# Kernel optimization log

Measured on AMD Instinct MI355X. Metric: run time of the kernel, lower is better.

Reference implementation:

```python
import jax, jax.numpy as jnp
import numpy as np

B, L, DIM, H, D, WS = 2, 2048, 1024, 16, 64, 256
SCALE = D ** -0.5


def _rope_tables(seq_len, dim, dtype):
    inv_freq = 1.0 / (10000.0 ** (jnp.arange(0, dim, 2, dtype=jnp.float32) / dim))
    t = jnp.arange(seq_len, dtype=jnp.float32)
    freqs = jnp.einsum('i,j->ij', t, inv_freq)          # [L, D/2]
    emb = jnp.concatenate([freqs, freqs], axis=-1)       # [L, D]
    return jnp.cos(emb).astype(dtype), jnp.sin(emb).astype(dtype)


def _rotate_half(x):
    x1, x2 = x[..., : x.shape[-1] // 2], x[..., x.shape[-1] // 2:]
    return jnp.concatenate([-x2, x1], axis=-1)


def _apply_rope(t, cos, sin):
    # t: [B, L, H, D]; cos/sin: [L, D] broadcast over batch and heads
    return t * cos[None, :, None, :] + _rotate_half(t) * sin[None, :, None, :]


def setup_inputs() -> dict:
    key = jax.random.key(0)
    k0, k1, k2 = jax.random.split(key, 3)
    x = jax.random.normal(k0, (B, L, DIM), dtype=jnp.float32)
    Wqkv = jax.random.normal(k1, (3 * H * D, DIM), dtype=jnp.float32) * 0.02
    bqkv = jnp.zeros((3 * H * D,), dtype=jnp.float32)
    Wproj = jax.random.normal(k2, (DIM, H * D), dtype=jnp.float32) * 0.02
    bproj = jnp.zeros((DIM,), dtype=jnp.float32)
    return {"x": x, "Wqkv": Wqkv, "bqkv": bqkv, "Wproj": Wproj, "bproj": bproj, "is_global": 1}


def _attention(x, Wqkv, bqkv, Wproj, bproj, is_global):
    b, l, _ = x.shape
    qkv = x @ Wqkv.T + bqkv                              # [B, L, 3*H*D]
    q, k, v = jnp.split(qkv, 3, axis=-1)
    q, k, v = (t.reshape(b, l, H, D) for t in (q, k, v))
    cos, sin = _rope_tables(l, D, x.dtype)
    q = _apply_rope(q, cos, sin)
    k = _apply_rope(k, cos, sin)
    if is_global:
        attn = jnp.einsum('bshd,bthd->bhst', q, k) * SCALE
        attn = jax.nn.softmax(attn, axis=-1)
        out = jnp.einsum('bhst,bthd->bshd', attn, v)     # [B, L, H, D]
    else:
        pad = (WS - l % WS) % WS
        if pad > 0:
            q, k, v = (jnp.pad(t, ((0, 0), (0, pad), (0, 0), (0, 0))) for t in (q, k, v))
        w = (l + pad) // WS
        q = q.reshape(b, w, WS, H, D)
        k = k.reshape(b, w, WS, H, D)
        v = v.reshape(b, w, WS, H, D)
        attn = jnp.einsum('bwshd,bwthd->bwhst', q, k) * SCALE
        attn = jax.nn.softmax(attn, axis=-1)
        out = jnp.einsum('bwhst,bwthd->bwshd', attn, v).reshape(b, w * WS, H, D)
        out = out[:, :l]
    return out.reshape(b, l, H * D) @ Wproj.T + bproj


def reference(x, Wqkv, bqkv, Wproj, bproj, is_global):
    return _attention(x, Wqkv, bqkv, Wproj, bproj, is_global)
```

## Files before the change

### kernel.cpp

```cpp
#include <hip/hip_runtime.h>
#include <math.h>

#define NB 2
#define NL 2048
#define NDIM 1024
#define NH 16
#define ND 64
#define NWS 256
#define NM (NB*NL)
#define QSCALE 0.18033688011112042f

typedef __attribute__((ext_vector_type(8))) short short8;
typedef __attribute__((ext_vector_type(4))) float f32x4;
typedef unsigned short ushort_t;
typedef unsigned int uint_t;

#define MFMA16(a,b,acc) __builtin_amdgcn_mfma_f32_16x16x32_bf16((a),(b),(acc),0,0,0)

static __device__ __forceinline__ ushort_t f2bf(float x){
    uint_t u = __float_as_uint(x);
    uint_t r = (u + 0x7fff + ((u >> 16) & 1)) >> 16;
    return (ushort_t)r;
}
static __device__ __forceinline__ float bf2f(ushort_t u){
    return __uint_as_float(((uint_t)u) << 16);
}
static __device__ __forceinline__ float fast_exp2(float x){
#if __has_builtin(__builtin_amdgcn_exp2f)
    return __builtin_amdgcn_exp2f(x);
#else
    return exp2f(x);
#endif
}

static __device__ __forceinline__ void async_load16(const void* g, void* l){
    __builtin_amdgcn_global_load_lds(
        (const __attribute__((address_space(1))) unsigned int*)g,
        (__attribute__((address_space(3))) unsigned int*)l, 16, 0, 0);
}

__launch_bounds__(256)
__global__ void split_all(const float* __restrict__ x,  ushort_t* __restrict__ xh,  ushort_t* __restrict__ xl,
                          const float* __restrict__ wq, ushort_t* __restrict__ wqh, ushort_t* __restrict__ wql,
                          const float* __restrict__ wp, ushort_t* __restrict__ wph, ushort_t* __restrict__ wpl)
{
    int i = blockIdx.x*256 + threadIdx.x;
    const float* in; ushort_t *oh, *ol;
    if (i < 1048576)      { in = x;  oh = xh;  ol = xl;  }
    else if (i < 1835008) { in = wq; oh = wqh; ol = wql; i -= 1048576; }
    else                  { in = wp; oh = wph; ol = wpl; i -= 1835008; }
    const int e = i*4;
    const float4 v = *(const float4*)(in + e);
    ushort_t h0=f2bf(v.x), h1=f2bf(v.y), h2=f2bf(v.z), h3=f2bf(v.w);
    ushort4 h4; h4.x=h0; h4.y=h1; h4.z=h2; h4.w=h3;
    ushort4 l4;
    l4.x=f2bf(v.x - bf2f(h0)); l4.y=f2bf(v.y - bf2f(h1));
    l4.z=f2bf(v.z - bf2f(h2)); l4.w=f2bf(v.w - bf2f(h3));
    *(ushort4*)(oh + e) = h4;
    *(ushort4*)(ol + e) = l4;
}

__launch_bounds__(256)
__global__ void rope_tab(float* __restrict__ tc, float* __restrict__ ts)
{
    const int idx = blockIdx.x*256 + threadIdx.x;
    const int j = idx >> 11, l = idx & (NL-1);
    const float invf = 1.0f / powf(10000.0f, (float)j * (1.0f/32.0f));
    float s, c;
    sincosf((float)l * invf, &s, &c);
    tc[idx] = c; ts[idx] = s;
}

__launch_bounds__(256, 3)
__global__ void gemm_qkv(const ushort_t* __restrict__ Ah, const ushort_t* __restrict__ Al,
                         const ushort_t* __restrict__ Bh,
                         const float* __restrict__ bias,
                         ushort_t* __restrict__ oQh, ushort_t* __restrict__ oKh,
                         ushort_t* __restrict__ oVth,
                         const float* __restrict__ tcos, const float* __restrict__ tsin)
{
    __shared__ __align__(16) char smem[50176];
    ushort_t* sA_h = (ushort_t*)smem;
    ushort_t* sA_l = (ushort_t*)(smem + 8192);
    ushort_t* sB_h = (ushort_t*)(smem + 16384);
    ushort_t* sBounce = (ushort_t*)smem;
    const int ebuf = 12288;
    const int bbuf = 24576;

    const int tid  = threadIdx.x;
    const int wv   = tid >> 6, lane = tid & 63;
    const int quad = lane >> 4, l16 = lane & 15;
    const int m0 = blockIdx.y << 7, n0 = blockIdx.x << 7;
    const int wr = wv >> 1, wc = wv & 1;

    const ushort_t* gsrc;
    ushort_t* lds_base;
    int rowb, npass;
    if (wv == 0)      { gsrc = Ah; lds_base = sA_h; rowb = m0; npass = 8; }
    else if (wv == 1) { gsrc = Al; lds_base = sA_l; rowb = m0; npass = 8; }
    else { gsrc = Bh; lds_base = sB_h + (wv-2)*64*32; rowb = n0 + (wv-2)*64; npass = 4; }
    const int rl = lane >> 2;
    const int cp = lane & 3;
    const int cg = cp ^ ((rl >> 1) & 3);
    const ushort_t* gptr = gsrc + (size_t)(rowb + rl)*NDIM + cg*8;

    f32x4 acc[4][4];
    #pragma unroll
    for (int i=0;i<4;++i)
        #pragma unroll
        for (int j=0;j<4;++j) acc[i][j] = (f32x4){0.f,0.f,0.f,0.f};

    const int swz = (l16 >> 1) & 3;
    const int ac_off = (wr*64 + l16)*32 + ((quad ^ swz) << 3);
    const int bc_off = (wc*64 + l16)*32 + ((quad ^ swz) << 3);

#define QSTAGE(BUF, KOFF) do { \
        const ushort_t* gp_ = gptr + (KOFF); \
        for (int p=0; p<npass; ++p) \
            async_load16(gp_ + (size_t)p*16*NDIM, (char*)lds_base + (BUF)*bbuf + p*1024); \
    } while(0)

#define QCOMP(BUF) do { \
        const int eo_ = (BUF)*ebuf; \
        short8 ah[4], al[4], bh[4]; \
        _Pragma("unroll") \
        for (int t=0;t<4;++t){ \
            ah[t] = *(const short8*)&sA_h[eo_ + t*512 + ac_off]; \
            al[t] = *(const short8*)&sA_l[eo_ + t*512 + ac_off]; \
            bh[t] = *(const short8*)&sB_h[eo_ + t*512 + bc_off]; \
        } \
        _Pragma("unroll") \
        for (int mt=0;mt<4;++mt) \
            _Pragma("unroll") \
            for (int nt=0;nt<4;++nt){ \
                f32x4 a_ = acc[mt][nt]; \
                a_ = MFMA16(ah[mt], bh[nt], a_); \
                a_ = MFMA16(al[mt], bh[nt], a_); \
                acc[mt][nt] = a_; \
            } \
    } while(0)

    QSTAGE(0, 0);
    for (int k0 = 0; k0 < NDIM; k0 += 64) {
        __syncthreads();
        QSTAGE(1, k0 + 32);
        QCOMP(0);
        __syncthreads();
        if (k0 + 64 < NDIM) QSTAGE(0, k0 + 64);
        QCOMP(1);
    }
#undef QSTAGE
#undef QCOMP

    const int colb = n0 + wc*64;
    const int sel  = colb >> 10;
    const int head = (colb & 1023) >> 6;
    float bq[4];
    #pragma unroll
    for (int nt=0;nt<4;++nt) bq[nt] = bias[colb + nt*16 + l16];

    if (sel == 2) {
        __syncthreads();
        const int bb = m0 >> 11;
        const int Lb = (m0 & (NL-1)) + wr*64;
        ushort_t* sT = sBounce + wv*(64*72);
        const size_t gb = ((size_t)(bb*NH + head)*ND)*NL + Lb;
        const int drow = lane >> 3, dcol = lane & 7;
        #pragma unroll
        for (int mt=0;mt<4;++mt)
            #pragma unroll
            for (int nt=0;nt<4;++nt)
                #pragma unroll
                for (int r=0;r<4;++r)
                    sT[(nt*16+l16)*72 + mt*16 + quad*4 + r] = f2bf(acc[mt][nt][r] + bq[nt]);
        #pragma unroll
        for (int dd=0; dd<8; ++dd){
            const int d = dd*8 + drow;
            const uint4 v = *(const uint4*)&sT[d*72 + dcol*8];
            *(uint4*)(oVth + gb + (size_t)d*NL + dcol*8) = v;
        }
    } else {
        ushort_t* dh = sel ? oKh : oQh;
        const float qs = sel ? 1.0f : QSCALE;
        #pragma unroll
        for (int mt=0;mt<4;++mt)
            #pragma unroll
            for (int r=0;r<4;++r){
                const int m = m0 + wr*64 + mt*16 + quad*4 + r;
                const int bb = m >> 11, l = m & (NL-1);
                const size_t ro = ((size_t)((bb*NH + head)*NL + l)) << 6;
                #pragma unroll
                for (int ntp=0;ntp<2;++ntp){
                    const int j = ntp*16 + l16;
                    const float c = tcos[j*NL + l];
                    const float s = tsin[j*NL + l];
                    const float x1 = acc[mt][ntp  ][r] + bq[ntp];
                    const float x2 = acc[mt][ntp+2][r] + bq[ntp+2];
                    const int d1 = ntp*16 + l16;
                    dh[ro + d1]      = f2bf((x1*c - x2*s) * qs);
                    dh[ro + d1 + 32] = f2bf((x2*c + x1*s) * qs);
                }
            }
    }
}

__launch_bounds__(256, 2)
__global__ void gemm_proj(const ushort_t* __restrict__ Ah, const ushort_t* __restrict__ Al,
                          const ushort_t* __restrict__ Bh, const ushort_t* __restrict__ Bl,
                          const float* __restrict__ bias,
                          float* __restrict__ Cout)
{
    __shared__ __align__(16) char smem[74752];
    ushort_t* sA_h = (ushort_t*)smem;
    ushort_t* sA_l = (ushort_t*)(smem + 8192);
    ushort_t* sB_h = (ushort_t*)(smem + 16384);
    ushort_t* sB_l = (ushort_t*)(smem + 20480);
    const int ebuf = 12288;
    const int bbuf = 24576;

    const int tid  = threadIdx.x;
    const int wv   = tid >> 6, lane = tid & 63;
    const int quad = lane >> 4, l16 = lane & 15;
    const int m0 = blockIdx.y << 7, n0 = blockIdx.x << 6;
    const int wr = wv >> 1, wc = wv & 1;

    const int rl = lane >> 2;
    const int cp = lane & 3;
    const int cg = cp ^ ((rl >> 1) & 3);
    const ushort_t* pAh = Ah + (size_t)(m0 + 32*wv + rl)*NDIM + cg*8;
    const ushort_t* pAl = Al + (size_t)(m0 + 32*wv + rl)*NDIM + cg*8;
    const ushort_t* pBh = Bh + (size_t)(n0 + 16*wv + rl)*NDIM + cg*8;
    const ushort_t* pBl = Bl + (size_t)(n0 + 16*wv + rl)*NDIM + cg*8;
    char* dA  = smem + wv*2048;
    char* dB0 = smem + 16384 + wv*1024;
    char* dB1 = smem + 20480 + wv*1024;

    f32x4 acc[4][2];
    #pragma unroll
    for (int i=0;i<4;++i)
        #pragma unroll
        for (int j=0;j<2;++j) acc[i][j] = (f32x4){0.f,0.f,0.f,0.f};

    const int swz = (l16 >> 1) & 3;
    const int ac_off = (wr*64 + l16)*32 + ((quad ^ swz) << 3);
    const int bc_off = (wc*32 + l16)*32 + ((quad ^ swz) << 3);

#define PSTAGE(SLOT, KOFF) do { \
        const int so_ = (SLOT)*bbuf; \
        async_load16(pAh + (KOFF),           dA + so_); \
        async_load16(pAh + 16*NDIM + (KOFF), dA + so_ + 1024); \
        async_load16(pAl + (KOFF),           dA + so_ + 8192); \
        async_load16(pAl + 16*NDIM + (KOFF), dA + so_ + 9216); \
        async_load16(pBh + (KOFF), dB0 + so_); \
        async_load16(pBl + (KOFF), dB1 + so_); \
    } while(0)

#define PCOMP(SLOT) do { \
        const int eo_ = (SLOT)*ebuf; \
        short8 ah[4], al[4], bh[2], bl[2]; \
        _Pragma("unroll") \
        for (int t=0;t<4;++t){ \
            ah[t] = *(const short8*)&sA_h[eo_ + t*512 + ac_off]; \
            al[t] = *(const short8*)&sA_l[eo_ + t*512 + ac_off]; \
        } \
        _Pragma("unroll") \
        for (int t=0;t<2;++t){ \
            bh[t] = *(const short8*)&sB_h[eo_ + t*512 + bc_off]; \
            bl[t] = *(const short8*)&sB_l[eo_ + t*512 + bc_off]; \
        } \
        _Pragma("unroll") \
        for (int mt=0;mt<4;++mt) \
            _Pragma("unroll") \
            for (int nt=0;nt<2;++nt){ \
                f32x4 a_ = acc[mt][nt]; \
                a_ = MFMA16(ah[mt], bh[nt], a_); \
                a_ = MFMA16(al[mt], bh[nt], a_); \
                a_ = MFMA16(ah[mt], bl[nt], a_); \
                acc[mt][nt] = a_; \
            } \
    } while(0)

#define PPHASE(SLOT, K0, VN) do { \
        asm volatile("s_waitcnt vmcnt(" #VN ")" ::: "memory"); \
        __builtin_amdgcn_sched_barrier(0); \
        __builtin_amdgcn_s_barrier(); \
        __builtin_amdgcn_sched_barrier(0); \
        PCOMP(SLOT); \
        asm volatile("s_waitcnt lgkmcnt(0)" ::: "memory"); \
        __builtin_amdgcn_sched_barrier(0); \
        __builtin_amdgcn_s_barrier(); \
        __builtin_amdgcn_sched_barrier(0); \
        if ((K0) + 96 < NDIM) PSTAGE(SLOT, (K0) + 96); \
    } while(0)

    PSTAGE(0, 0); PSTAGE(1, 32); PSTAGE(2, 64);
    for (int k0 = 0; k0 < 960; k0 += 96) {
        PPHASE(0, k0,      12);
        PPHASE(1, k0 + 32, 12);
        PPHASE(2, k0 + 64, 12);
    }
    PPHASE(0, 960, 0);
    PPHASE(1, 992, 0);
#undef PSTAGE
#undef PCOMP
#undef PPHASE

    const int colb = n0 + wc*32;
    float bq[2];
    #pragma unroll
    for (int nt=0;nt<2;++nt) bq[nt] = bias[colb + nt*16 + l16];
    #pragma unroll
    for (int mt=0;mt<4;++mt)
        #pragma unroll
        for (int r=0;r<4;++r){
            const int m = m0 + wr*64 + mt*16 + quad*4 + r;
            float* orow = Cout + (size_t)m*NDIM + colb;
            #pragma unroll
            for (int nt=0;nt<2;++nt)
                orow[nt*16 + l16] = acc[mt][nt][r] + bq[nt];
        }
}

__launch_bounds__(256, 4)
__global__ void attn_mfma(const ushort_t* __restrict__ Qh,
                          const ushort_t* __restrict__ Kh,
                          const ushort_t* __restrict__ Vth,
                          ushort_t* __restrict__ AOh, ushort_t* __restrict__ AOl,
                          const int* __restrict__ isg)
{
    __shared__ __align__(16) char smem[40960];

    const int tid  = threadIdx.x;
    const int wv   = tid >> 6, lane = tid & 63;
    const int quad = lane >> 4, l16 = lane & 15;
    const int bh = blockIdx.x & 31, qt = blockIdx.x >> 5;
    const int q0w = qt*64 + wv*16;

    short8 bq0, bq1;
    {
        const size_t rb = (((size_t)bh*NL + q0w) << 6) + (size_t)(l16 << 6) + quad*8;
        bq0 = *(const short8*)(Qh + rb);
        bq1 = *(const short8*)(Qh + rb + 32);
    }
    short8 ones;
    #pragma unroll
    for (int j=0;j<8;++j) ones[j] = (short)0x3F80;

    f32x4 o[4];
    #pragma unroll
    for (int dnt=0; dnt<4; ++dnt) o[dnt] = (f32x4){0.f,0.f,0.f,0.f};
    f32x4 lsacc = (f32x4){0.f,0.f,0.f,0.f};

    const int gflag = isg[0];
    int klo, khi;
    if (gflag) { klo = 0; khi = NL; }
    else       { klo = (qt >> 2)*NWS; khi = klo + NWS; }

    const int swz4 = (l16 & 7) << 4;
    const int KC0 = l16*128 + (( quad*16      ) ^ swz4);
    const int KC1 = l16*128 + (( quad*16 + 64 ) ^ swz4);
    const int sPb = 32768 + wv*2048;
    int PW[4];
    #pragma unroll
    for (int knt=0; knt<4; ++knt)
        PW[knt] = sPb + l16*128 + ((knt*32 + quad*8) ^ swz4);
    const int PR0 = sPb + KC0;
    const int PR1 = sPb + KC1;

    const int r8  = lane >> 3;
    const int c8s = (lane & 7) ^ r8;
    const ushort_t* Kp = Kh + (((size_t)bh*NL) << 6)
                       + (size_t)(klo + wv*16 + r8)*64 + c8s*8;
    const ushort_t* Vp = Vth + (size_t)bh*ND*NL
                       + (size_t)(wv*16 + r8)*NL + klo + c8s*8;
    const int kdst = wv*2048;
    const int vdst = 16384 + wv*2048;

#define STAGE(BUF) do { \
        async_load16(Kp,          smem + (BUF)*8192 + kdst); \
        async_load16(Kp + 512,    smem + (BUF)*8192 + kdst + 1024); \
        async_load16(Vp,          smem + (BUF)*8192 + vdst); \
        async_load16(Vp + 8*NL,   smem + (BUF)*8192 + vdst + 1024); \
        Kp += 64*64; Vp += 64; } while (0)

#define TILE(BUF) do { \
        const char* kb_ = smem + (BUF)*8192; \
        const char* vb_ = smem + 16384 + (BUF)*8192; \
        f32x4 s_[4]; \
        _Pragma("unroll") \
        for (int knt=0; knt<4; ++knt) { \
            const short8 a0 = *(const short8*)(kb_ + knt*2048 + KC0); \
            const short8 a1 = *(const short8*)(kb_ + knt*2048 + KC1); \
            f32x4 t = (f32x4){0.f,0.f,0.f,0.f}; \
            t = MFMA16(a0, bq0, t); \
            t = MFMA16(a1, bq1, t); \
            s_[knt] = t; \
        } \
        _Pragma("unroll") \
        for (int knt=0; knt<4; ++knt) { \
            const uint_t u0 = __float_as_uint(fast_exp2(s_[knt][0])); \
            const uint_t u1 = __float_as_uint(fast_exp2(s_[knt][1])); \
            const uint_t u2 = __float_as_uint(fast_exp2(s_[knt][2])); \
            const uint_t u3 = __float_as_uint(fast_exp2(s_[knt][3])); \
            uint2 pk_; \
            pk_.x = __builtin_amdgcn_perm(u1, u0, 0x07060302u); \
            pk_.y = __builtin_amdgcn_perm(u3, u2, 0x07060302u); \
            *(uint2*)(smem + PW[knt]) = pk_; \
        } \
        const short8 fp0 = *(const short8*)(smem + PR0); \
        const short8 fp1 = *(const short8*)(smem + PR1); \
        lsacc = MFMA16(fp0, ones, lsacc); \
        lsacc = MFMA16(fp1, ones, lsacc); \
        _Pragma("unroll") \
        for (int dnt=0; dnt<4; ++dnt) { \
            const short8 v0 = *(const short8*)(vb_ + dnt*2048 + KC0); \
            const short8 v1 = *(const short8*)(vb_ + dnt*2048 + KC1); \
            f32x4 t = o[dnt]; \
            t = MFMA16(fp0, v0, t); \
            t = MFMA16(fp1, v1, t); \
            o[dnt] = t; \
        } } while (0)

    STAGE(0);
    for (int kt = klo; kt < khi; kt += 128) {
        __syncthreads();
        if (kt + 64 < khi) STAGE(1);
        TILE(0);
        __syncthreads();
        if (kt + 128 < khi) STAGE(0);
        TILE(1);
    }
#undef STAGE
#undef TILE

    const int bb = bh >> 4, hh = bh & 15;
    #pragma unroll
    for (int r=0; r<4; ++r) {
        const float inv = 1.0f / lsacc[r];
        const int row = q0w + quad*4 + r;
        const size_t ob = (((size_t)(bb*NL + row)) << 10) + (hh << 6);
        #pragma unroll
        for (int dnt=0; dnt<4; ++dnt) {
            const float val = o[dnt][r] * inv;
            const ushort_t h = f2bf(val);
            AOh[ob + dnt*16 + l16] = h;
            AOl[ob + dnt*16 + l16] = f2bf(val - bf2f(h));
        }
    }
}

extern "C" void kernel_launch(void* const* d_in, const int* in_sizes, int n_in,
                              void* d_out, int out_size, void* d_ws, size_t ws_size,
                              hipStream_t stream)
{
    const float* x     = (const float*)d_in[0];
    const float* Wqkv  = (const float*)d_in[1];
    const float* bqkv  = (const float*)d_in[2];
    const float* Wproj = (const float*)d_in[3];
    const float* bproj = (const float*)d_in[4];
    const int*   isg   = (const int*)d_in[5];
    float* out = (float*)d_out;
    char* base = (char*)d_ws;

    const size_t MB = 1024*1024;
    ushort_t* Qh  = (ushort_t*)(base);
    ushort_t* Kh  = (ushort_t*)(base + 16*MB);
    ushort_t* Vth = (ushort_t*)(base + 32*MB);
    ushort_t* xh  = (ushort_t*)(base + 48*MB);
    ushort_t* xl  = (ushort_t*)(base + 56*MB);
    ushort_t* AOh = xh;
    ushort_t* AOl = xl;
    ushort_t* Wqh = (ushort_t*)(base + 64*MB);
    ushort_t* Wql = (ushort_t*)(base + 64*MB + 6291456);
    ushort_t* Wph = (ushort_t*)(base + 76*MB);
    ushort_t* Wpl = (ushort_t*)(base + 76*MB + 2097152);
    float*    tcs = (float*)(base + 80*MB);
    float*    tsn = (float*)(base + 80*MB + 262144);

    split_all<<<8192, 256, 0, stream>>>(x, xh, xl, Wqkv, Wqh, Wql, Wproj, Wph, Wpl);
    rope_tab<<<256, 256, 0, stream>>>(tcs, tsn);

    gemm_qkv<<<dim3(3*NDIM/128, NM/128), 256, 0, stream>>>(
        xh, xl, Wqh, bqkv, Qh, Kh, Vth, tcs, tsn);

    attn_mfma<<<NB*NH*(NL/64), 256, 0, stream>>>(
        Qh, Kh, Vth, AOh, AOl, isg);

    gemm_proj<<<dim3(NDIM/64, NM/128), 256, 0, stream>>>(
        AOh, AOl, Wph, Wpl, bproj, out);
}
```

Measured before the change: 223.3 us.

## Process two 16-row query tiles per wave in attention kernel

Each wave now handles 32 query rows (two MFMA M-tiles) instead of 16, so each block covers 128 queries and the grid is halved. Every K/V tile staged into shared memory is reused across twice as many queries, which halves global K/V traffic and LDS reads per query. In exchange the kernel needs more registers and more shared memory for the P buffers, so occupancy drops (launch bounds go from 4 to 3). With half as many blocks there may also be fewer blocks than needed to keep the GPU full.

```diff
diff --git a/kernel.cpp b/kernel.cpp
--- a/kernel.cpp
+++ b/kernel.cpp
@@ -321,45 +321,51 @@
         }
 }
 
-__launch_bounds__(256, 4)
+__launch_bounds__(256, 3)
 __global__ void attn_mfma(const ushort_t* __restrict__ Qh,
                           const ushort_t* __restrict__ Kh,
                           const ushort_t* __restrict__ Vth,
                           ushort_t* __restrict__ AOh, ushort_t* __restrict__ AOl,
                           const int* __restrict__ isg)
 {
-    __shared__ __align__(16) char smem[40960];
+    __shared__ __align__(16) char smem[49152];
 
     const int tid  = threadIdx.x;
     const int wv   = tid >> 6, lane = tid & 63;
     const int quad = lane >> 4, l16 = lane & 15;
     const int bh = blockIdx.x & 31, qt = blockIdx.x >> 5;
-    const int q0w = qt*64 + wv*16;
-
-    short8 bq0, bq1;
+    const int q0w = qt*128 + wv*32;
+
+    short8 bq[2][2];
     {
-        const size_t rb = (((size_t)bh*NL + q0w) << 6) + (size_t)(l16 << 6) + quad*8;
-        bq0 = *(const short8*)(Qh + rb);
-        bq1 = *(const short8*)(Qh + rb + 32);
+        const size_t rb = (((size_t)bh*NL + q0w) << 6);
+        #pragma unroll
+        for (int mt=0; mt<2; ++mt)
+            #pragma unroll
+            for (int c=0; c<2; ++c)
+                bq[mt][c] = *(const short8*)(Qh + rb + (size_t)((mt*16 + l16) << 6) + quad*8 + c*32);
     }
     short8 ones;
     #pragma unroll
     for (int j=0;j<8;++j) ones[j] = (short)0x3F80;
 
-    f32x4 o[4];
-    #pragma unroll
-    for (int dnt=0; dnt<4; ++dnt) o[dnt] = (f32x4){0.f,0.f,0.f,0.f};
-    f32x4 lsacc = (f32x4){0.f,0.f,0.f,0.f};
+    f32x4 o[2][4];
+    #pragma unroll
+    for (int mt=0; mt<2; ++mt)
+        #pragma unroll
+        for (int dnt=0; dnt<4; ++dnt)
+            o[mt][dnt] = (f32x4){0.f,0.f,0.f,0.f};
+    f32x4 lsacc[2] = {(f32x4){0.f,0.f,0.f,0.f}, (f32x4){0.f,0.f,0.f,0.f}};
 
     const int gflag = isg[0];
     int klo, khi;
     if (gflag) { klo = 0; khi = NL; }
-    else       { klo = (qt >> 2)*NWS; khi = klo + NWS; }
+    else       { klo = (qt >> 1)*NWS; khi = klo + NWS; }
 
     const int swz4 = (l16 & 7) << 4;
     const int KC0 = l16*128 + (( quad*16      ) ^ swz4);
     const int KC1 = l16*128 + (( quad*16 + 64 ) ^ swz4);
-    const int sPb = 32768 + wv*2048;
+    const int sPb = 32768 + wv*4096;
     int PW[4];
     #pragma unroll
     for (int knt=0; knt<4; ++knt)
@@ -386,39 +392,51 @@
 #define TILE(BUF) do { \
         const char* kb_ = smem + (BUF)*8192; \
         const char* vb_ = smem + 16384 + (BUF)*8192; \
-        f32x4 s_[4]; \
+        f32x4 s0_[4], s1_[4]; \
         _Pragma("unroll") \
         for (int knt=0; knt<4; ++knt) { \
             const short8 a0 = *(const short8*)(kb_ + knt*2048 + KC0); \
             const short8 a1 = *(const short8*)(kb_ + knt*2048 + KC1); \
-            f32x4 t = (f32x4){0.f,0.f,0.f,0.f}; \
-            t = MFMA16(a0, bq0, t); \
-            t = MFMA16(a1, bq1, t); \
-            s_[knt] = t; \
+            f32x4 t0 = (f32x4){0.f,0.f,0.f,0.f}; \
+            t0 = MFMA16(a0, bq[0][0], t0); \
+            t0 = MFMA16(a1, bq[0][1], t0); \
+            s0_[knt] = t0; \
+            f32x4 t1 = (f32x4){0.f,0.f,0.f,0.f}; \
+            t1 = MFMA16(a0, bq[1][0], t1); \
+            t1 = MFMA16(a1, bq[1][1], t1); \
+            s1_[knt] = t1; \
         } \
-        _Pragma("unroll") \
-        for (int knt=0; knt<4; ++knt) { \
-            const uint_t u0 = __float_as_uint(fast_exp2(s_[knt][0])); \
-            const uint_t u1 = __float_as_uint(fast_exp2(s_[knt][1])); \
-            const uint_t u2 = __float_as_uint(fast_exp2(s_[knt][2])); \
-            const uint_t u3 = __float_as_uint(fast_exp2(s_[knt][3])); \
-            uint2 pk_; \
-            pk_.x = __builtin_amdgcn_perm(u1, u0, 0x07060302u); \
-            pk_.y = __builtin_amdgcn_perm(u3, u2, 0x07060302u); \
-            *(uint2*)(smem + PW[knt]) = pk_; \
+        short8 fp[2][2]; \
+        _Pragma("unroll") \
+        for (int mt=0; mt<2; ++mt) { \
+            _Pragma("unroll") \
+            for (int knt=0; knt<4; ++knt) { \
+                const f32x4 sv = mt ? s1_[knt] : s0_[knt]; \
+                const uint_t u0 = __float_as_uint(fast_exp2(sv[0])); \
+                const uint_t u1 = __float_as_uint(fast_exp2(sv[1])); \
+                const uint_t u2 = __float_as_uint(fast_exp2(sv[2])); \
+                const uint_t u3 = __float_as_uint(fast_exp2(sv[3])); \
+                uint2 pk_; \
+                pk_.x = __builtin_amdgcn_perm(u1, u0, 0x07060302u); \
+                pk_.y = __builtin_amdgcn_perm(u3, u2, 0x07060302u); \
+                *(uint2*)(smem + mt*2048 + PW[knt]) = pk_; \
+            } \
+            fp[mt][0] = *(const short8*)(smem + mt*2048 + PR0); \
+            fp[mt][1] = *(const short8*)(smem + mt*2048 + PR1); \
+            lsacc[mt] = MFMA16(fp[mt][0], ones, lsacc[mt]); \
+            lsacc[mt] = MFMA16(fp[mt][1], ones, lsacc[mt]); \
         } \
-        const short8 fp0 = *(const short8*)(smem + PR0); \
-        const short8 fp1 = *(const short8*)(smem + PR1); \
-        lsacc = MFMA16(fp0, ones, lsacc); \
-        lsacc = MFMA16(fp1, ones, lsacc); \
         _Pragma("unroll") \
         for (int dnt=0; dnt<4; ++dnt) { \
             const short8 v0 = *(const short8*)(vb_ + dnt*2048 + KC0); \
             const short8 v1 = *(const short8*)(vb_ + dnt*2048 + KC1); \
-            f32x4 t = o[dnt]; \
-            t = MFMA16(fp0, v0, t); \
-            t = MFMA16(fp1, v1, t); \
-            o[dnt] = t; \
+            _Pragma("unroll") \
+            for (int mt=0; mt<2; ++mt) { \
+                f32x4 t = o[mt][dnt]; \
+                t = MFMA16(fp[mt][0], v0, t); \
+                t = MFMA16(fp[mt][1], v1, t); \
+                o[mt][dnt] = t; \
+            } \
         } } while (0)
 
     STAGE(0);
@@ -435,18 +453,20 @@
 
     const int bb = bh >> 4, hh = bh & 15;
     #pragma unroll
-    for (int r=0; r<4; ++r) {
-        const float inv = 1.0f / lsacc[r];
-        const int row = q0w + quad*4 + r;
-        const size_t ob = (((size_t)(bb*NL + row)) << 10) + (hh << 6);
-        #pragma unroll
-        for (int dnt=0; dnt<4; ++dnt) {
-            const float val = o[dnt][r] * inv;
-            const ushort_t h = f2bf(val);
-            AOh[ob + dnt*16 + l16] = h;
-            AOl[ob + dnt*16 + l16] = f2bf(val - bf2f(h));
+    for (int mt=0; mt<2; ++mt)
+        #pragma unroll
+        for (int r=0; r<4; ++r) {
+            const float inv = 1.0f / lsacc[mt][r];
+            const int row = q0w + mt*16 + quad*4 + r;
+            const size_t ob = (((size_t)(bb*NL + row)) << 10) + (hh << 6);
+            #pragma unroll
+            for (int dnt=0; dnt<4; ++dnt) {
+                const float val = o[mt][dnt][r] * inv;
+                const ushort_t h = f2bf(val);
+                AOh[ob + dnt*16 + l16] = h;
+                AOl[ob + dnt*16 + l16] = f2bf(val - bf2f(h));
+            }
         }
-    }
 }
 
 extern "C" void kernel_launch(void* const* d_in, const int* in_sizes, int n_in,
@@ -483,7 +503,7 @@
     gemm_qkv<<<dim3(3*NDIM/128, NM/128), 256, 0, stream>>>(
         xh, xl, Wqh, bqkv, Qh, Kh, Vth, tcs, tsn);
 
-    attn_mfma<<<NB*NH*(NL/64), 256, 0, stream>>>(
+    attn_mfma<<<NB*NH*(NL/128), 256, 0, stream>>>(
         Qh, Kh, Vth, AOh, AOl, isg);
 
     gemm_proj<<<dim3(NDIM/64, NM/128), 256, 0, stream>>>(
```

After: 212.7 us. -4.8%, faster.
